# Kernel tuning notes

Hardware: AMD Instinct MI355X
Metric: run time of the kernel (lower is better)

## Reference

```python
import jax, jax.numpy as jnp
import numpy as np

N = 50000      # nodes
E = 800000     # edges per meta-path
P = 3          # meta-paths
IN = 128       # in_size
H = 8          # heads
D = 32         # out_size per head
EMB = 128      # embedding_dim


def setup_inputs() -> dict:
    key = jax.random.key(0)
    ks = jax.random.split(key, 7)
    h = jax.random.normal(ks[0], (N, IN), jnp.float32)
    edge_index = jax.random.randint(ks[1], (P, 2, E), 0, N, dtype=jnp.int32)
    fc_w = jax.random.normal(ks[2], (P, IN, H * D), jnp.float32) * 0.05
    attn_l = jax.random.normal(ks[3], (P, H, D), jnp.float32) * 0.1
    attn_r = jax.random.normal(ks[4], (P, H, D), jnp.float32) * 0.1
    sem_w = jax.random.normal(ks[5], (P * H * D, EMB), jnp.float32) * 0.05
    sem_b = jnp.zeros((EMB,), jnp.float32)
    return {"h": h, "edge_index": edge_index, "fc_w": fc_w,
            "attn_l": attn_l, "attn_r": attn_r, "sem_w": sem_w, "sem_b": sem_b}


def _gat(h, W, al, ar, src, dst):
    # DGL GATConv (no bias/residual), eval mode (no dropout)
    feat = (h @ W).reshape(N, H, D)                      # (N,H,D)
    el = jnp.einsum('nhd,hd->nh', feat, al)              # (N,H)
    er = jnp.einsum('nhd,hd->nh', feat, ar)
    e = jax.nn.leaky_relu(el[src] + er[dst], negative_slope=0.2)  # (E,H)
    # edge softmax over incoming edges of each dst node
    m = jax.ops.segment_max(e, dst, num_segments=N)      # (N,H); -inf only for empty segs (never indexed)
    ex = jnp.exp(e - m[dst])
    den = jax.ops.segment_sum(ex, dst, num_segments=N)   # (N,H)
    a = ex / den[dst]                                    # (E,H)
    msg = feat[src] * a[..., None]                       # (E,H,D) gather + weight
    out = jax.ops.segment_sum(msg, dst, num_segments=N)  # (N,H,D) scatter-add
    return jax.nn.elu(out).reshape(N, H * D)             # flatten(1)


def reference(h, edge_index, fc_w, attn_l, attn_r, sem_w, sem_b):
    src = edge_index[:, 0]  # (P,E)
    dst = edge_index[:, 1]
    # run one GATConv per meta-path, vectorized over the meta-path axis
    z = jax.vmap(_gat, in_axes=(None, 0, 0, 0, 0, 0))(h, fc_w, attn_l, attn_r, src, dst)  # (P,N,H*D)
    z = jnp.transpose(z, (1, 0, 2)).reshape(N, P * H * D)  # stack(dim=1) then reshape [N,-1]
    return z @ sem_w + sem_b                                # SemanticAttention.project2
```

## Files before the change

### kernel.cpp

```cpp
#include <hip/hip_runtime.h>
#include <hip/hip_bf16.h>

#define N_NODES 50000
#define N_EDGES 800000
#define NPATH 3
#define NBKT 196
#define NBKT3 (NPATH * NBKT)
#define NCHUNKBLK 256
#define CHUNK 9375
#define LDS_STRIDE 260

typedef __attribute__((ext_vector_type(8))) short short8;
typedef __attribute__((ext_vector_type(4))) float v4f;

__device__ __forceinline__ short f2bf(float v, float* back) {
  unsigned u = __float_as_uint(v);
  unsigned r = (u + 0x7FFFu + ((u >> 16) & 1u)) >> 16;
  *back = __uint_as_float(r << 16);
  return (short)r;
}

__device__ __forceinline__ float bfu(unsigned x) {
  return __uint_as_float(x << 16);
}

__global__ __launch_bounds__(256) void blk_count_kernel(
    const int* __restrict__ ei, int* __restrict__ cntmat) {
  __shared__ int lcnt[NBKT3];
  const int t = threadIdx.x, blk = blockIdx.x;
  for (int j = t; j < NBKT3; j += 256) lcnt[j] = 0;
  __syncthreads();
  const int lo = blk * CHUNK, hi = lo + CHUNK;
  for (int idx = lo + t; idx < hi; idx += 256) {
    int p = idx / N_EDGES, e = idx - p * N_EDGES;
    int d = ei[p * 2 * N_EDGES + N_EDGES + e];
    atomicAdd(&lcnt[p * NBKT + (d >> 8)], 1);
  }
  __syncthreads();
  for (int j = t; j < NBKT3; j += 256) cntmat[blk * NBKT3 + j] = lcnt[j];
}

__global__ __launch_bounds__(256) void col_scan_kernel(
    const int* __restrict__ cntmat, int* __restrict__ pos, int* __restrict__ btot) {
  __shared__ int tmp[256];
  const int b = blockIdx.x, t = threadIdx.x;
  int v = cntmat[t * NBKT3 + b];
  tmp[t] = v;
  __syncthreads();
  for (int ofs = 1; ofs < 256; ofs <<= 1) {
    int x = (t >= ofs) ? tmp[t - ofs] : 0;
    __syncthreads();
    tmp[t] += x;
    __syncthreads();
  }
  pos[b * 256 + t] = tmp[t] - v;
  if (t == 255) btot[b] = tmp[255];
}

__global__ __launch_bounds__(1024) void bucket_scan_kernel(
    const int* __restrict__ btot, int* __restrict__ boff) {
  __shared__ int tmp[1024];
  const int t = threadIdx.x;
  int v = (t < NBKT3) ? btot[t] : 0;
  tmp[t] = v;
  __syncthreads();
  for (int ofs = 1; ofs < 1024; ofs <<= 1) {
    int x = (t >= ofs) ? tmp[t - ofs] : 0;
    __syncthreads();
    tmp[t] += x;
    __syncthreads();
  }
  if (t < NBKT3) boff[t] = tmp[t] - v;
}

__global__ __launch_bounds__(256) void scatter_det_kernel(
    const int* __restrict__ ei, const int* __restrict__ boff,
    const int* __restrict__ pos, int2* __restrict__ ebuf) {
  __shared__ int cursor[NBKT3];
  const int t = threadIdx.x, blk = blockIdx.x;
  for (int j = t; j < NBKT3; j += 256)
    cursor[j] = boff[j] + pos[j * 256 + blk];
  __syncthreads();
  const int lo = blk * CHUNK, hi = lo + CHUNK;
  for (int idx = lo + t; idx < hi; idx += 256) {
    int p = idx / N_EDGES, e = idx - p * N_EDGES;
    int s = ei[p * 2 * N_EDGES + e];
    int d = ei[p * 2 * N_EDGES + N_EDGES + e];
    int ps = atomicAdd(&cursor[p * NBKT + (d >> 8)], 1);
    ebuf[ps] = make_int2(s, d);
  }
}

__global__ __launch_bounds__(256) void bucket_csr_kernel(
    const int2* __restrict__ ebuf, const int* __restrict__ boff,
    const int* __restrict__ btot,
    int* __restrict__ off3, int* __restrict__ deg3, int* __restrict__ csr_src) {
  __shared__ int cnt[256], excl[256], cur[256];
  const int b = blockIdx.x;
  const int t = threadIdx.x;
  const int p = b / NBKT;
  const int node_base = (b - p * NBKT) * 256;
  const int start = boff[b];
  const int ecount = btot[b];

  cnt[t] = 0;
  __syncthreads();
  for (int i = t; i < ecount; i += 256)
    atomicAdd(&cnt[ebuf[start + i].y & 255], 1);
  __syncthreads();

  int v = cnt[t];
  excl[t] = v;
  __syncthreads();
  for (int ofs = 1; ofs < 256; ofs <<= 1) {
    int x = (t >= ofs) ? excl[t - ofs] : 0;
    __syncthreads();
    excl[t] += x;
    __syncthreads();
  }
  int my_excl = excl[t] - v;
  cur[t] = my_excl;
  const int node = node_base + t;
  if (node < N_NODES) {
    off3[p * N_NODES + node] = start + my_excl;
    deg3[p * N_NODES + node] = v;
  }
  __syncthreads();

  for (int i = t; i < ecount; i += 256) {
    int2 e = ebuf[start + i];
    int pos2 = atomicAdd(&cur[e.y & 255], 1);
    csr_src[start + pos2] = e.x;
  }
}

__global__ __launch_bounds__(256) void prep_kernel(
    const float* __restrict__ fc_w, const float* __restrict__ attn_l,
    const float* __restrict__ attn_r, const float* __restrict__ sem_w,
    __hip_bfloat16* __restrict__ Wf_hi, __hip_bfloat16* __restrict__ Wf_lo,
    __hip_bfloat16* __restrict__ Bs_hi, __hip_bfloat16* __restrict__ Bs_lo) {
  const int p = blockIdx.x / 33;
  const int unit = blockIdx.x % 33;
  const int t = threadIdx.x;
  if (unit < 17) {
    const float* W = fc_w + (size_t)p * 128 * 256;
    int idx = unit * 256 + t;
    int lane = idx & 63;
    int tmp = idx >> 6;
    int nt = tmp % 17, kc = tmp / 17;
    int l15 = lane & 15, quad = lane >> 4;
    __hip_bfloat16* oh = Wf_hi + (size_t)p * 34816;
    __hip_bfloat16* ol = Wf_lo + (size_t)p * 34816;
    for (int j = 0; j < 8; j++) {
      int k = kc * 32 + quad * 8 + j;
      float v;
      if (nt < 16) {
        v = W[k * 256 + nt * 16 + l15];
      } else {
        int h8 = l15 & 7;
        const float* av = ((l15 < 8) ? attn_l : attn_r) + (size_t)p * 256 + h8 * 32;
        v = 0.f;
        for (int dd = 0; dd < 32; dd++)
          v = fmaf(W[k * 256 + h8 * 32 + dd], av[dd], v);
      }
      float back, back2;
      short hb = f2bf(v, &back);
      short lb = f2bf(v - back, &back2);
      ((short*)oh)[(tmp * 64 + lane) * 8 + j] = hb;
      ((short*)ol)[(tmp * 64 + lane) * 8 + j] = lb;
    }
  } else {
    const float* Ws = sem_w + (size_t)p * 256 * 128;
    int idx = (unit - 17) * 256 + t;
    int lane = idx & 63;
    int tmp = idx >> 6;
    int nt = tmp & 7, kc = tmp >> 3;
    int l15 = lane & 15, quad = lane >> 4;
    __hip_bfloat16* oh = Bs_hi + (size_t)p * 32768;
    __hip_bfloat16* ol = Bs_lo + (size_t)p * 32768;
    for (int j = 0; j < 8; j++) {
      int k = kc * 32 + quad * 8 + j;
      float v = Ws[k * 128 + nt * 16 + l15];
      float back, back2;
      short hb = f2bf(v, &back);
      short lb = f2bf(v - back, &back2);
      ((short*)oh)[(tmp * 64 + lane) * 8 + j] = hb;
      ((short*)ol)[(tmp * 64 + lane) * 8 + j] = lb;
    }
  }
}

__global__ __launch_bounds__(64) void feat_mfma_kernel(
    const float* __restrict__ h,
    const __hip_bfloat16* __restrict__ Wf_hi_all,
    const __hip_bfloat16* __restrict__ Wf_lo_all,
    __hip_bfloat16* __restrict__ feat3, float* __restrict__ el3,
    float* __restrict__ er3) {
  const int p = blockIdx.y;
  const __hip_bfloat16* Wf_hi = Wf_hi_all + (size_t)p * 34816;
  const __hip_bfloat16* Wf_lo = Wf_lo_all + (size_t)p * 34816;
  __hip_bfloat16* feat = feat3 + (size_t)p * N_NODES * 256;
  float* el = el3 + (size_t)p * N_NODES * 8;
  float* er = er3 + (size_t)p * N_NODES * 8;

  const int lane = threadIdx.x;
  const int l15 = lane & 15, quad = lane >> 4;
  const int m0 = blockIdx.x * 16;
  const int mrow = m0 + l15;

  v4f acc[17];
#pragma unroll
  for (int nt = 0; nt < 17; nt++) acc[nt] = {0.f, 0.f, 0.f, 0.f};

#pragma unroll
  for (int kc = 0; kc < 4; kc++) {
    const float* hrow = h + (size_t)mrow * 128 + kc * 32 + quad * 8;
    float4 fa = *(const float4*)hrow;
    float4 fb = *(const float4*)(hrow + 4);
    float fv[8] = {fa.x, fa.y, fa.z, fa.w, fb.x, fb.y, fb.z, fb.w};
    short8 ahi, alo;
#pragma unroll
    for (int q = 0; q < 8; q++) {
      float back, back2;
      ahi[q] = f2bf(fv[q], &back);
      alo[q] = f2bf(fv[q] - back, &back2);
    }
#pragma unroll
    for (int nt = 0; nt < 17; nt++) {
      const int o = ((kc * 17 + nt) * 64 + lane) * 8;
      short8 bhi = *(const short8*)(Wf_hi + o);
      short8 blo = *(const short8*)(Wf_lo + o);
      acc[nt] = __builtin_amdgcn_mfma_f32_16x16x32_bf16(ahi, bhi, acc[nt], 0, 0, 0);
      acc[nt] = __builtin_amdgcn_mfma_f32_16x16x32_bf16(ahi, blo, acc[nt], 0, 0, 0);
      acc[nt] = __builtin_amdgcn_mfma_f32_16x16x32_bf16(alo, bhi, acc[nt], 0, 0, 0);
    }
  }

#pragma unroll
  for (int nt = 0; nt < 16; nt++)
#pragma unroll
    for (int r = 0; r < 4; r++) {
      int m = m0 + quad * 4 + r;
      feat[(size_t)m * 256 + nt * 16 + l15] = __float2bfloat16(acc[nt][r]);
    }
#pragma unroll
  for (int r = 0; r < 4; r++) {
    int m = m0 + quad * 4 + r;
    float v = acc[16][r];
    if (l15 < 8) el[m * 8 + l15] = v;
    else         er[m * 8 + (l15 - 8)] = v;
  }
}

__device__ __forceinline__ void edge8(
    const int* __restrict__ lst, int j, const float* __restrict__ el,
    float erh, const ushort* __restrict__ fp, int lane, int hh,
    float& aD, float& aN0, float& aN1, float& aN2, float& aN3) {
  int s[8];
#pragma unroll
  for (int k = 0; k < 8; k++) s[k] = lst[j + k];
  float x[8];
  ushort4 f[8];
#pragma unroll
  for (int k = 0; k < 8; k++) {
    x[k] = el[s[k] * 8 + hh];
    f[k] = *(const ushort4*)(fp + (size_t)s[k] * 256 + lane * 4);
  }
#pragma unroll
  for (int k = 0; k < 8; k++) {
    float xx = x[k] + erh;
    xx = xx > 0.f ? xx : 0.2f * xx;
    float e = __expf(xx);
    aD += e;
    aN0 = fmaf(e, bfu(f[k].x), aN0);
    aN1 = fmaf(e, bfu(f[k].y), aN1);
    aN2 = fmaf(e, bfu(f[k].z), aN2);
    aN3 = fmaf(e, bfu(f[k].w), aN3);
  }
}

__device__ __forceinline__ void edge4(
    const int* __restrict__ lst, int j, const float* __restrict__ el,
    float erh, const ushort* __restrict__ fp, int lane, int hh,
    float& aD, float& aN0, float& aN1, float& aN2, float& aN3) {
  int s[4];
#pragma unroll
  for (int k = 0; k < 4; k++) s[k] = lst[j + k];
  float x[4];
  ushort4 f[4];
#pragma unroll
  for (int k = 0; k < 4; k++) {
    x[k] = el[s[k] * 8 + hh];
    f[k] = *(const ushort4*)(fp + (size_t)s[k] * 256 + lane * 4);
  }
#pragma unroll
  for (int k = 0; k < 4; k++) {
    float xx = x[k] + erh;
    xx = xx > 0.f ? xx : 0.2f * xx;
    float e = __expf(xx);
    aD += e;
    aN0 = fmaf(e, bfu(f[k].x), aN0);
    aN1 = fmaf(e, bfu(f[k].y), aN1);
    aN2 = fmaf(e, bfu(f[k].z), aN2);
    aN3 = fmaf(e, bfu(f[k].w), aN3);
  }
}

__device__ __forceinline__ void edge1(
    const int* __restrict__ lst, int j, const float* __restrict__ el,
    float erh, const ushort* __restrict__ fp, int lane, int hh,
    float& aD, float& aN0, float& aN1, float& aN2, float& aN3) {
  int s = lst[j];
  float x = el[s * 8 + hh] + erh;
  ushort4 f0 = *(const ushort4*)(fp + (size_t)s * 256 + lane * 4);
  x = x > 0.f ? x : 0.2f * x;
  float e0 = __expf(x);
  aD += e0;
  aN0 = fmaf(e0, bfu(f0.x), aN0);
  aN1 = fmaf(e0, bfu(f0.y), aN1);
  aN2 = fmaf(e0, bfu(f0.z), aN2);
  aN3 = fmaf(e0, bfu(f0.w), aN3);
}

__global__ __launch_bounds__(512) void agg_sem_kernel(
    const int* __restrict__ csr_src, const int* __restrict__ off,
    const int* __restrict__ deg,
    const float* __restrict__ el, const float* __restrict__ er,
    const __hip_bfloat16* __restrict__ feat,
    const __hip_bfloat16* __restrict__ Bs_hi, const __hip_bfloat16* __restrict__ Bs_lo,
    const float* __restrict__ bias, float* __restrict__ out, int mode) {
  __shared__ float Arow[16 * LDS_STRIDE];
  const int t = threadIdx.x;
  const int w = t >> 6, lane = t & 63;
  const int hh = lane >> 3;
  const int node_base = blockIdx.x * 16;
  const ushort* fp = (const ushort*)feat;

#pragma unroll
  for (int i = 0; i < 2; i++) {
    const int node = node_base + 2 * w + i;
    const int n = deg[node];
    const int* lst = csr_src + off[node];
    const float erh = er[node * 8 + hh];

    float aN0 = 0.f, aN1 = 0.f, aN2 = 0.f, aN3 = 0.f, aD = 0.f;
    int j = 0;
    for (; j + 8 <= n; j += 8)
      edge8(lst, j, el, erh, fp, lane, hh, aD, aN0, aN1, aN2, aN3);
    if (j + 4 <= n) {
      edge4(lst, j, el, erh, fp, lane, hh, aD, aN0, aN1, aN2, aN3);
      j += 4;
    }
    for (; j < n; j++)
      edge1(lst, j, el, erh, fp, lane, hh, aD, aN0, aN1, aN2, aN3);

    float inv = (n > 0) ? 1.f / aD : 0.f;
    float r0 = aN0 * inv, r1 = aN1 * inv, r2 = aN2 * inv, r3 = aN3 * inv;
    r0 = r0 > 0.f ? r0 : (__expf(r0) - 1.f);
    r1 = r1 > 0.f ? r1 : (__expf(r1) - 1.f);
    r2 = r2 > 0.f ? r2 : (__expf(r2) - 1.f);
    r3 = r3 > 0.f ? r3 : (__expf(r3) - 1.f);
    *(float4*)&Arow[(2 * w + i) * LDS_STRIDE + lane * 4] =
        make_float4(r0, r1, r2, r3);
  }
  __syncthreads();

  const int nt = w;
  const int l15 = lane & 15, quad = lane >> 4;
  v4f acc = {0.f, 0.f, 0.f, 0.f};
#pragma unroll
  for (int kc = 0; kc < 8; kc++) {
    const float* ap = &Arow[l15 * LDS_STRIDE + kc * 32 + quad * 8];
    float4 a0 = *(const float4*)ap;
    float4 a1 = *(const float4*)(ap + 4);
    float fv[8] = {a0.x, a0.y, a0.z, a0.w, a1.x, a1.y, a1.z, a1.w};
    short8 ahi, alo;
#pragma unroll
    for (int q = 0; q < 8; q++) {
      float back, back2;
      ahi[q] = f2bf(fv[q], &back);
      alo[q] = f2bf(fv[q] - back, &back2);
    }
    const int o = ((kc * 8 + nt) * 64 + lane) * 8;
    short8 bhi = *(const short8*)(Bs_hi + o);
    short8 blo = *(const short8*)(Bs_lo + o);
    acc = __builtin_amdgcn_mfma_f32_16x16x32_bf16(ahi, bhi, acc, 0, 0, 0);
    acc = __builtin_amdgcn_mfma_f32_16x16x32_bf16(ahi, blo, acc, 0, 0, 0);
    acc = __builtin_amdgcn_mfma_f32_16x16x32_bf16(alo, bhi, acc, 0, 0, 0);
  }

#pragma unroll
  for (int r = 0; r < 4; r++) {
    int m = node_base + quad * 4 + r;
    size_t o = (size_t)m * 128 + nt * 16 + l15;
    float v = acc[r];
    if (mode == 0) v += bias[nt * 16 + l15];
    else           v += out[o];
    out[o] = v;
  }
}

extern "C" void kernel_launch(void* const* d_in, const int* in_sizes, int n_in,
                              void* d_out, int out_size, void* d_ws, size_t ws_size,
                              hipStream_t stream) {
  const float* h      = (const float*)d_in[0];
  const int*   ei     = (const int*)d_in[1];
  const float* fc_w   = (const float*)d_in[2];
  const float* attn_l = (const float*)d_in[3];
  const float* attn_r = (const float*)d_in[4];
  const float* sem_w  = (const float*)d_in[5];
  const float* sem_b  = (const float*)d_in[6];
  float* out = (float*)d_out;

  char* ws = (char*)d_ws;
  __hip_bfloat16* feat3 = (__hip_bfloat16*)ws;
  float* el3     = (float*)(ws + 76800000);
  float* er3     = (float*)(ws + 81600000);
  int*   csr_src = (int*)(ws + 86400000);
  int2*  ebuf    = (int2*)(ws + 96000000);
  int*   deg3    = (int*)(ws + 115200000);
  int*   off3    = (int*)(ws + 115800000);
  int*   cntmat  = (int*)(ws + 116400000);
  int*   posm    = (int*)(ws + 117050000);
  int*   btot    = (int*)(ws + 117700000);
  int*   boff    = (int*)(ws + 117710000);
  __hip_bfloat16* Wf_hi = (__hip_bfloat16*)(ws + 117800000);
  __hip_bfloat16* Wf_lo = (__hip_bfloat16*)(ws + 118050000);
  __hip_bfloat16* Bs_hi = (__hip_bfloat16*)(ws + 118300000);
  __hip_bfloat16* Bs_lo = (__hip_bfloat16*)(ws + 118550000);

  blk_count_kernel<<<NCHUNKBLK, 256, 0, stream>>>(ei, cntmat);
  col_scan_kernel<<<NBKT3, 256, 0, stream>>>(cntmat, posm, btot);
  bucket_scan_kernel<<<1, 1024, 0, stream>>>(btot, boff);
  scatter_det_kernel<<<NCHUNKBLK, 256, 0, stream>>>(ei, boff, posm, ebuf);
  bucket_csr_kernel<<<NBKT3, 256, 0, stream>>>(ebuf, boff, btot, off3, deg3, csr_src);
  prep_kernel<<<NPATH * 33, 256, 0, stream>>>(fc_w, attn_l, attn_r, sem_w,
                                              Wf_hi, Wf_lo, Bs_hi, Bs_lo);

  feat_mfma_kernel<<<dim3(N_NODES / 16, NPATH), 64, 0, stream>>>(
      h, Wf_hi, Wf_lo, feat3, el3, er3);

  for (int p = 0; p < NPATH; p++) {
    agg_sem_kernel<<<N_NODES / 16, 512, 0, stream>>>(
        csr_src, off3 + p * N_NODES, deg3 + p * N_NODES,
        el3 + (size_t)p * N_NODES * 8, er3 + (size_t)p * N_NODES * 8,
        feat3 + (size_t)p * N_NODES * 256,
        Bs_hi + (size_t)p * 32768, Bs_lo + (size_t)p * 32768,
        sem_b, out, p);
  }
}
```

Baseline: 493.1 us.

## Split wave into edge-parallel halves with 16-byte feature gathers and precomputed bf16 split

The aggregation wave now handles two edges at once. Each 32-lane half processes alternate edges, gathers 8 bf16 features per lane with a single 16-byte load, and the halves are combined with a cross-lane shuffle. The hi/lo bf16 split of the ELU output is computed once in the aggregation phase and stored in LDS as bf16, so the MFMA phase no longer converts from fp32. This aims to raise memory-level parallelism on the gathers and remove redundant conversion work, at the cost of more registers and a predicated tail loop.

```diff
diff --git a/kernel.cpp b/kernel.cpp
--- a/kernel.cpp
+++ b/kernel.cpp
@@ -8,7 +8,7 @@
 #define NBKT3 (NPATH * NBKT)
 #define NCHUNKBLK 256
 #define CHUNK 9375
-#define LDS_STRIDE 260
+#define A_STR 264
 
 typedef __attribute__((ext_vector_type(8))) short short8;
 typedef __attribute__((ext_vector_type(4))) float v4f;
@@ -20,8 +20,11 @@
   return (short)r;
 }
 
-__device__ __forceinline__ float bfu(unsigned x) {
-  return __uint_as_float(x << 16);
+__device__ __forceinline__ float bflo(unsigned u) {
+  return __uint_as_float(u << 16);
+}
+__device__ __forceinline__ float bfhi(unsigned u) {
+  return __uint_as_float(u & 0xFFFF0000u);
 }
 
 __global__ __launch_bounds__(256) void blk_count_kernel(
@@ -252,76 +255,6 @@
   }
 }
 
-__device__ __forceinline__ void edge8(
-    const int* __restrict__ lst, int j, const float* __restrict__ el,
-    float erh, const ushort* __restrict__ fp, int lane, int hh,
-    float& aD, float& aN0, float& aN1, float& aN2, float& aN3) {
-  int s[8];
-#pragma unroll
-  for (int k = 0; k < 8; k++) s[k] = lst[j + k];
-  float x[8];
-  ushort4 f[8];
-#pragma unroll
-  for (int k = 0; k < 8; k++) {
-    x[k] = el[s[k] * 8 + hh];
-    f[k] = *(const ushort4*)(fp + (size_t)s[k] * 256 + lane * 4);
-  }
-#pragma unroll
-  for (int k = 0; k < 8; k++) {
-    float xx = x[k] + erh;
-    xx = xx > 0.f ? xx : 0.2f * xx;
-    float e = __expf(xx);
-    aD += e;
-    aN0 = fmaf(e, bfu(f[k].x), aN0);
-    aN1 = fmaf(e, bfu(f[k].y), aN1);
-    aN2 = fmaf(e, bfu(f[k].z), aN2);
-    aN3 = fmaf(e, bfu(f[k].w), aN3);
-  }
-}
-
-__device__ __forceinline__ void edge4(
-    const int* __restrict__ lst, int j, const float* __restrict__ el,
-    float erh, const ushort* __restrict__ fp, int lane, int hh,
-    float& aD, float& aN0, float& aN1, float& aN2, float& aN3) {
-  int s[4];
-#pragma unroll
-  for (int k = 0; k < 4; k++) s[k] = lst[j + k];
-  float x[4];
-  ushort4 f[4];
-#pragma unroll
-  for (int k = 0; k < 4; k++) {
-    x[k] = el[s[k] * 8 + hh];
-    f[k] = *(const ushort4*)(fp + (size_t)s[k] * 256 + lane * 4);
-  }
-#pragma unroll
-  for (int k = 0; k < 4; k++) {
-    float xx = x[k] + erh;
-    xx = xx > 0.f ? xx : 0.2f * xx;
-    float e = __expf(xx);
-    aD += e;
-    aN0 = fmaf(e, bfu(f[k].x), aN0);
-    aN1 = fmaf(e, bfu(f[k].y), aN1);
-    aN2 = fmaf(e, bfu(f[k].z), aN2);
-    aN3 = fmaf(e, bfu(f[k].w), aN3);
-  }
-}
-
-__device__ __forceinline__ void edge1(
-    const int* __restrict__ lst, int j, const float* __restrict__ el,
-    float erh, const ushort* __restrict__ fp, int lane, int hh,
-    float& aD, float& aN0, float& aN1, float& aN2, float& aN3) {
-  int s = lst[j];
-  float x = el[s * 8 + hh] + erh;
-  ushort4 f0 = *(const ushort4*)(fp + (size_t)s * 256 + lane * 4);
-  x = x > 0.f ? x : 0.2f * x;
-  float e0 = __expf(x);
-  aD += e0;
-  aN0 = fmaf(e0, bfu(f0.x), aN0);
-  aN1 = fmaf(e0, bfu(f0.y), aN1);
-  aN2 = fmaf(e0, bfu(f0.z), aN2);
-  aN3 = fmaf(e0, bfu(f0.w), aN3);
-}
-
 __global__ __launch_bounds__(512) void agg_sem_kernel(
     const int* __restrict__ csr_src, const int* __restrict__ off,
     const int* __restrict__ deg,
@@ -329,39 +262,94 @@
     const __hip_bfloat16* __restrict__ feat,
     const __hip_bfloat16* __restrict__ Bs_hi, const __hip_bfloat16* __restrict__ Bs_lo,
     const float* __restrict__ bias, float* __restrict__ out, int mode) {
-  __shared__ float Arow[16 * LDS_STRIDE];
+  __shared__ __align__(16) short Ahi[16 * A_STR];
+  __shared__ __align__(16) short Alo[16 * A_STR];
   const int t = threadIdx.x;
   const int w = t >> 6, lane = t & 63;
-  const int hh = lane >> 3;
+  const int half = lane >> 5;
+  const int l5 = lane & 31;
+  const int hh = l5 >> 2;
   const int node_base = blockIdx.x * 16;
   const ushort* fp = (const ushort*)feat;
+  const ushort* fpl = fp + l5 * 8;
+  const float* elh = el + hh;
 
 #pragma unroll
   for (int i = 0; i < 2; i++) {
     const int node = node_base + 2 * w + i;
     const int n = deg[node];
-    const int* lst = csr_src + off[node];
+    const int* lst = csr_src + off[node] + half;
     const float erh = er[node * 8 + hh];
 
-    float aN0 = 0.f, aN1 = 0.f, aN2 = 0.f, aN3 = 0.f, aD = 0.f;
+    float aN[8] = {0.f, 0.f, 0.f, 0.f, 0.f, 0.f, 0.f, 0.f};
+    float aD = 0.f;
     int j = 0;
-    for (; j + 8 <= n; j += 8)
-      edge8(lst, j, el, erh, fp, lane, hh, aD, aN0, aN1, aN2, aN3);
-    if (j + 4 <= n) {
-      edge4(lst, j, el, erh, fp, lane, hh, aD, aN0, aN1, aN2, aN3);
-      j += 4;
-    }
-    for (; j < n; j++)
-      edge1(lst, j, el, erh, fp, lane, hh, aD, aN0, aN1, aN2, aN3);
+    for (; j + 8 <= n; j += 8) {
+      int s0 = lst[j + 0], s1 = lst[j + 2], s2 = lst[j + 4], s3 = lst[j + 6];
+      unsigned u0 = (unsigned)s0, u1 = (unsigned)s1,
+               u2 = (unsigned)s2, u3 = (unsigned)s3;
+      float x0 = elh[(size_t)u0 * 8], x1 = elh[(size_t)u1 * 8],
+            x2 = elh[(size_t)u2 * 8], x3 = elh[(size_t)u3 * 8];
+      uint4 f0 = *(const uint4*)(fpl + (size_t)u0 * 256);
+      uint4 f1 = *(const uint4*)(fpl + (size_t)u1 * 256);
+      uint4 f2 = *(const uint4*)(fpl + (size_t)u2 * 256);
+      uint4 f3 = *(const uint4*)(fpl + (size_t)u3 * 256);
+#pragma unroll
+      for (int u = 0; u < 4; u++) {
+        float x = (u == 0) ? x0 : (u == 1) ? x1 : (u == 2) ? x2 : x3;
+        uint4 f = (u == 0) ? f0 : (u == 1) ? f1 : (u == 2) ? f2 : f3;
+        float xx = x + erh;
+        xx = xx > 0.f ? xx : 0.2f * xx;
+        float e = __expf(xx);
+        aD += e;
+        aN[0] = fmaf(e, bflo(f.x), aN[0]);
+        aN[1] = fmaf(e, bfhi(f.x), aN[1]);
+        aN[2] = fmaf(e, bflo(f.y), aN[2]);
+        aN[3] = fmaf(e, bfhi(f.y), aN[3]);
+        aN[4] = fmaf(e, bflo(f.z), aN[4]);
+        aN[5] = fmaf(e, bfhi(f.z), aN[5]);
+        aN[6] = fmaf(e, bflo(f.w), aN[6]);
+        aN[7] = fmaf(e, bfhi(f.w), aN[7]);
+      }
+    }
+    for (; j < n; j += 2) {
+      int v = (j + half) < n;
+      int s_ = lst[v ? j : j - 1];
+      unsigned su = (unsigned)s_;
+      float x = elh[(size_t)su * 8];
+      uint4 f = *(const uint4*)(fpl + (size_t)su * 256);
+      float xx = x + erh;
+      xx = xx > 0.f ? xx : 0.2f * xx;
+      float e = v ? __expf(xx) : 0.f;
+      aD += e;
+      aN[0] = fmaf(e, bflo(f.x), aN[0]);
+      aN[1] = fmaf(e, bfhi(f.x), aN[1]);
+      aN[2] = fmaf(e, bflo(f.y), aN[2]);
+      aN[3] = fmaf(e, bfhi(f.y), aN[3]);
+      aN[4] = fmaf(e, bflo(f.z), aN[4]);
+      aN[5] = fmaf(e, bfhi(f.z), aN[5]);
+      aN[6] = fmaf(e, bflo(f.w), aN[6]);
+      aN[7] = fmaf(e, bfhi(f.w), aN[7]);
+    }
+
+#pragma unroll
+    for (int k = 0; k < 8; k++) aN[k] += __shfl_xor(aN[k], 32, 64);
+    aD += __shfl_xor(aD, 32, 64);
 
     float inv = (n > 0) ? 1.f / aD : 0.f;
-    float r0 = aN0 * inv, r1 = aN1 * inv, r2 = aN2 * inv, r3 = aN3 * inv;
-    r0 = r0 > 0.f ? r0 : (__expf(r0) - 1.f);
-    r1 = r1 > 0.f ? r1 : (__expf(r1) - 1.f);
-    r2 = r2 > 0.f ? r2 : (__expf(r2) - 1.f);
-    r3 = r3 > 0.f ? r3 : (__expf(r3) - 1.f);
-    *(float4*)&Arow[(2 * w + i) * LDS_STRIDE + lane * 4] =
-        make_float4(r0, r1, r2, r3);
+    short8 hi8, lo8;
+#pragma unroll
+    for (int k = 0; k < 8; k++) {
+      float r = aN[k] * inv;
+      r = r > 0.f ? r : (__expf(r) - 1.f);
+      float back, back2;
+      hi8[k] = f2bf(r, &back);
+      lo8[k] = f2bf(r - back, &back2);
+    }
+    const int row = 2 * w + i;
+    short* dst = half ? Alo : Ahi;
+    short8 vv = half ? lo8 : hi8;
+    *(short8*)&dst[row * A_STR + l5 * 8] = vv;
   }
   __syncthreads();
 
@@ -370,17 +358,8 @@
   v4f acc = {0.f, 0.f, 0.f, 0.f};
 #pragma unroll
   for (int kc = 0; kc < 8; kc++) {
-    const float* ap = &Arow[l15 * LDS_STRIDE + kc * 32 + quad * 8];
-    float4 a0 = *(const float4*)ap;
-    float4 a1 = *(const float4*)(ap + 4);
-    float fv[8] = {a0.x, a0.y, a0.z, a0.w, a1.x, a1.y, a1.z, a1.w};
-    short8 ahi, alo;
-#pragma unroll
-    for (int q = 0; q < 8; q++) {
-      float back, back2;
-      ahi[q] = f2bf(fv[q], &back);
-      alo[q] = f2bf(fv[q] - back, &back2);
-    }
+    short8 ahi = *(const short8*)&Ahi[l15 * A_STR + kc * 32 + quad * 8];
+    short8 alo = *(const short8*)&Alo[l15 * A_STR + kc * 32 + quad * 8];
     const int o = ((kc * 8 + nt) * 64 + lane) * 8;
     short8 bhi = *(const short8*)(Bs_hi + o);
     short8 blo = *(const short8*)(Bs_lo + o);
```

Result: no change. 501.3 us (+1.7%).
